# Performance work log

Measured on AMD Instinct MI355X. Metric: run time of the kernel, lower is better.

The kernel has to match this reference:

```python
import jax, jax.numpy as jnp
import numpy as np

N, E, F, ED, H, G = 100000, 400000, 143, 6, 128, 4096
NL = 3   # num_layers -> NL-1 atom GATConv layers
NT = 2   # num_timesteps


def leaky(v):
    return jnp.where(v >= 0, v, 0.01 * v)  # torch default negative_slope=0.01


def gru_cell(xin, hid, Wi, Wh, bi, bh):
    # torch.nn.GRUCell, gate order r,z,n
    gi = xin @ Wi.T + bi
    gh = hid @ Wh.T + bh
    ir, iz, inn = jnp.split(gi, 3, axis=-1)
    hr, hz, hn = jnp.split(gh, 3, axis=-1)
    r = jax.nn.sigmoid(ir + hr)
    z = jax.nn.sigmoid(iz + hz)
    n = jnp.tanh(inn + r * hn)
    return (1.0 - z) * n + z * hid


def seg_softmax(a, seg, num):
    m = jax.ops.segment_max(a, seg, num_segments=num)
    m = jnp.where(jnp.isfinite(m), m, 0.0)
    e = jnp.exp(a - m[seg])
    s = jax.ops.segment_sum(e, seg, num_segments=num)
    return e / (s[seg] + 1e-16)


def afp_forward(x, edge_attr, lin1_W, lin1_b, gc_lin1_W, gc_att_l, gc_att_r,
                gc_lin2_W, gc_bias, gru0_Wi, gru0_Wh, gru0_bi, gru0_bh,
                atom_W, atom_att_src, atom_att_dst, atom_bias,
                atom_gru_Wi, atom_gru_Wh, atom_gru_bi, atom_gru_bh,
                mol_W, mol_att_src, mol_att_dst, mol_bias,
                mol_gru_Wi, mol_gru_Wh, mol_gru_bi, mol_gru_bh,
                lin2_W, lin2_b, cls_W1, cls_b1, cls_W2, cls_b2,
                edge_index, batch, num_graphs):
    src, dst = edge_index[0], edge_index[1]
    Nn = x.shape[0]
    # lin1 + leaky_relu
    x0 = leaky(x @ lin1_W.T + lin1_b)                                  # [N,H]
    # GATEConv (edge-feature gated attention)
    t = leaky(jnp.concatenate([x0[src], edge_attr], axis=-1) @ gc_lin1_W.T)  # [E,H]
    alpha = leaky(t @ gc_att_l + (x0 @ gc_att_r)[dst])                 # [E]
    alpha = seg_softmax(alpha, dst, Nn)
    x2 = x0 @ gc_lin2_W.T
    agg = jax.ops.segment_sum(x2[src] * alpha[:, None], dst, num_segments=Nn) + gc_bias
    h = jax.nn.elu(agg)
    xh = jax.nn.relu(gru_cell(h, x0, gru0_Wi, gru0_Wh, gru0_bi, gru0_bh))
    # atom GATConv layers (single head, no self loops, slope 0.01)
    for l in range(atom_W.shape[0]):
        xl = xh @ atom_W[l].T                                          # [N,H]
        a = leaky((xl @ atom_att_src[l])[src] + (xl @ atom_att_dst[l])[dst])
        a = seg_softmax(a, dst, Nn)
        agg = jax.ops.segment_sum(xl[src] * a[:, None], dst, num_segments=Nn) + atom_bias[l]
        h = jax.nn.elu(agg)
        xh = jax.nn.relu(gru_cell(h, xh, atom_gru_Wi[l], atom_gru_Wh[l], atom_gru_bi[l], atom_gru_bh[l]))
    # molecule readout: bipartite GATConv node->graph + GRU, NT timesteps
    out = jax.nn.relu(jax.ops.segment_sum(xh, batch, num_segments=num_graphs))  # [G,H]
    xm = xh @ mol_W.T
    a_src = xm @ mol_att_src                                           # [N]
    for _ in range(NT):
        om = out @ mol_W.T
        a = leaky(a_src + (om @ mol_att_dst)[batch])
        a = seg_softmax(a, batch, num_graphs)
        agg = jax.ops.segment_sum(xm * a[:, None], batch, num_segments=num_graphs) + mol_bias
        h = jax.nn.elu(agg)
        out = jax.nn.relu(gru_cell(h, out, mol_gru_Wi, mol_gru_Wh, mol_gru_bi, mol_gru_bh))
    emb = out @ lin2_W.T + lin2_b                                      # [G,H]
    y = jax.nn.relu(emb @ cls_W1.T + cls_b1) @ cls_W2.T + cls_b2       # [G,1]
    return y[:, 0]


def setup_inputs():
    key = jax.random.key(0)
    ks = iter(jax.random.split(key, 64))
    def rn(shape, s=0.08):
        return jax.random.normal(next(ks), shape, dtype=jnp.float32) * s
    return dict(
        x=jax.random.normal(next(ks), (N, F), dtype=jnp.float32),
        edge_attr=jax.random.normal(next(ks), (E, ED), dtype=jnp.float32),
        lin1_W=rn((H, F)), lin1_b=rn((H,)),
        gc_lin1_W=rn((H, H + ED)), gc_att_l=rn((H,)), gc_att_r=rn((H,)),
        gc_lin2_W=rn((H, H)), gc_bias=rn((H,)),
        gru0_Wi=rn((3 * H, H)), gru0_Wh=rn((3 * H, H)), gru0_bi=rn((3 * H,)), gru0_bh=rn((3 * H,)),
        atom_W=rn((NL - 1, H, H)), atom_att_src=rn((NL - 1, H)), atom_att_dst=rn((NL - 1, H)), atom_bias=rn((NL - 1, H)),
        atom_gru_Wi=rn((NL - 1, 3 * H, H)), atom_gru_Wh=rn((NL - 1, 3 * H, H)),
        atom_gru_bi=rn((NL - 1, 3 * H)), atom_gru_bh=rn((NL - 1, 3 * H)),
        mol_W=rn((H, H)), mol_att_src=rn((H,)), mol_att_dst=rn((H,)), mol_bias=rn((H,)),
        mol_gru_Wi=rn((3 * H, H)), mol_gru_Wh=rn((3 * H, H)), mol_gru_bi=rn((3 * H,)), mol_gru_bh=rn((3 * H,)),
        lin2_W=rn((H, H)), lin2_b=rn((H,)),
        cls_W1=rn((64, H)), cls_b1=rn((64,)), cls_W2=rn((1, 64)), cls_b2=rn((1,)),
        edge_index=jax.random.randint(next(ks), (2, E), 0, N),
        batch=jnp.sort(jax.random.randint(next(ks), (N,), 0, G)),
        num_graphs=G,
    )


def reference(x, edge_attr, lin1_W, lin1_b, gc_lin1_W, gc_att_l, gc_att_r,
              gc_lin2_W, gc_bias, gru0_Wi, gru0_Wh, gru0_bi, gru0_bh,
              atom_W, atom_att_src, atom_att_dst, atom_bias,
              atom_gru_Wi, atom_gru_Wh, atom_gru_bi, atom_gru_bh,
              mol_W, mol_att_src, mol_att_dst, mol_bias,
              mol_gru_Wi, mol_gru_Wh, mol_gru_bi, mol_gru_bh,
              lin2_W, lin2_b, cls_W1, cls_b1, cls_W2, cls_b2,
              edge_index, batch, num_graphs):
    return afp_forward(x, edge_attr, lin1_W, lin1_b, gc_lin1_W, gc_att_l, gc_att_r,
                       gc_lin2_W, gc_bias, gru0_Wi, gru0_Wh, gru0_bi, gru0_bh,
                       atom_W, atom_att_src, atom_att_dst, atom_bias,
                       atom_gru_Wi, atom_gru_Wh, atom_gru_bi, atom_gru_bh,
                       mol_W, mol_att_src, mol_att_dst, mol_bias,
                       mol_gru_Wi, mol_gru_Wh, mol_gru_bi, mol_gru_bh,
                       lin2_W, lin2_b, cls_W1, cls_b1, cls_W2, cls_b2,
                       edge_index, batch, num_graphs)
```

## Files before the change

kernel.cpp:

```cpp
#include <hip/hip_runtime.h>

#define NND 100000
#define NED 400000
#define FEAT 143
#define FEATP 160
#define EDIM 6
#define H 128
#define NG 4096
#define NBS 391

typedef __attribute__((ext_vector_type(8))) short bf8;
typedef __attribute__((ext_vector_type(4))) float f4;

__device__ __forceinline__ float b2f(unsigned short u){
  unsigned int x = ((unsigned int)u) << 16;
  return __builtin_bit_cast(float, x);
}
__device__ __forceinline__ unsigned short f2b(float f){
  unsigned int u = __builtin_bit_cast(unsigned int, f);
  u = u + 0x7fffu + ((u >> 16) & 1u);
  return (unsigned short)(u >> 16);
}
__device__ __forceinline__ float lk(float v){ return v >= 0.f ? v : 0.01f*v; }
__device__ __forceinline__ float eluf(float v){ return v > 0.f ? v : __expf(v) - 1.f; }
__device__ __forceinline__ float sgm(float v){ return 1.f/(1.f + __expf(-v)); }
__device__ __forceinline__ float wsum(float v){
  #pragma unroll
  for(int o=32;o>0;o>>=1) v += __shfl_xor(v,o);
  return v;
}
__device__ __forceinline__ bf8 cvt8(const float* p){
  f4 a = *(const f4*)p;
  f4 b = *(const f4*)(p+4);
  bf8 t;
  t[0]=(short)f2b(a[0]); t[1]=(short)f2b(a[1]); t[2]=(short)f2b(a[2]); t[3]=(short)f2b(a[3]);
  t[4]=(short)f2b(b[0]); t[5]=(short)f2b(b[1]); t[6]=(short)f2b(b[2]); t[7]=(short)f2b(b[3]);
  return t;
}

__global__ __launch_bounds__(256) void k_wfrag(const float* __restrict__ src, int lds, int srcK,
                                               unsigned short* __restrict__ dst, int NT, int KB){
  int i = blockIdx.x*256 + threadIdx.x;
  int total = NT*KB*512;
  if (i >= total) return;
  int j = i & 7, lane = (i>>3) & 63, kb = (i>>9) % KB, nt = i/(KB*512);
  int n = nt*16 + (lane & 15), k = kb*32 + (lane>>4)*8 + j;
  dst[i] = (k < srcK) ? f2b(src[(size_t)n*lds + k]) : (unsigned short)0;
}

__global__ __launch_bounds__(256) void k_hist(const int* __restrict__ ei, int* __restrict__ deg){
  int e = blockIdx.x*256 + threadIdx.x;
  if (e < NED) atomicAdd(&deg[ei[NED + e]], 1);
}
__global__ __launch_bounds__(256) void k_scan1(const int* __restrict__ deg, int* __restrict__ off, int* __restrict__ bsum){
  __shared__ int s[256];
  int i = blockIdx.x*256 + threadIdx.x;
  int v = (i < NND) ? deg[i] : 0;
  s[threadIdx.x] = v; __syncthreads();
  for(int o=1;o<256;o<<=1){
    int t = 0; if (threadIdx.x >= o) t = s[threadIdx.x - o];
    __syncthreads(); s[threadIdx.x] += t; __syncthreads();
  }
  if (i < NND) off[i] = s[threadIdx.x] - v;
  if (threadIdx.x == 255) bsum[blockIdx.x] = s[255];
}
__global__ __launch_bounds__(512) void k_scan2(int* __restrict__ bsum){
  __shared__ int s[512];
  int t = threadIdx.x;
  int v = (t < NBS) ? bsum[t] : 0;
  s[t] = v; __syncthreads();
  for(int o=1;o<512;o<<=1){
    int x = 0; if (t >= o) x = s[t - o];
    __syncthreads(); s[t] += x; __syncthreads();
  }
  if (t < NBS) bsum[t] = s[t] - v;
  if (t == 511) bsum[NBS] = s[511];
}
__global__ __launch_bounds__(256) void k_scan3(int* __restrict__ off, const int* __restrict__ bsum, int* __restrict__ cursor){
  int i = blockIdx.x*256 + threadIdx.x;
  if (i < NND){
    int v = off[i] + bsum[blockIdx.x];
    off[i] = v; cursor[i] = v;
  }
  if (i == 0) off[NND] = bsum[NBS];
}
__global__ __launch_bounds__(256) void k_scatter(const int* __restrict__ ei, int* __restrict__ cursor, int* __restrict__ perm){
  int e = blockIdx.x*256 + threadIdx.x;
  if (e < NED){
    int p = atomicAdd(&cursor[ei[NED + e]], 1);
    perm[p] = e;
  }
}
__global__ __launch_bounds__(256) void k_gstart(const int* __restrict__ batch, int* __restrict__ goff){
  int i = blockIdx.x*256 + threadIdx.x;
  if (i >= NND) return;
  int bi = batch[i];
  int bp = (i > 0) ? batch[i-1] : -1;
  for(int g = bp+1; g <= bi; g++) goff[g] = i;
  if (i == NND-1) for(int g = bi+1; g <= NG; g++) goff[g] = NND;
}

__global__ __launch_bounds__(256) void k_padx(const float* __restrict__ x, unsigned short* __restrict__ xp){
  int r = blockIdx.x*4 + (threadIdx.x >> 6);
  int lane = threadIdx.x & 63;
  if (r >= NND) return;
  for(int i = lane; i < FEATP; i += 64)
    xp[(size_t)r*FEATP + i] = (i < FEAT) ? f2b(x[(size_t)r*FEAT + i]) : (unsigned short)0;
}

template<int KB, int RT, bool ABF16, bool BIAS, int ACT, bool OBF16>
__global__ __launch_bounds__(256) void k_gemm(const void* __restrict__ Ap, int lda,
        const unsigned short* __restrict__ Wf,
        const float* __restrict__ bias, void* __restrict__ Cp, int M)
{
  int tid = threadIdx.x, wave = tid >> 6, lane = tid & 63;
  int m = lane & 15, quad = lane >> 4;
  int r0 = blockIdx.x * (16*RT);
  bf8 a[RT][KB];
  #pragma unroll
  for(int rt=0; rt<RT; rt++){
    int row = r0 + rt*16 + m;
    if (ABF16){
      const unsigned short* base = (const unsigned short*)Ap + (size_t)row*lda + quad*8;
      #pragma unroll
      for(int kb=0;kb<KB;kb++) a[rt][kb] = *(const bf8*)(base + kb*32);
    } else {
      const float* base = (const float*)Ap + (size_t)row*lda + quad*8;
      #pragma unroll
      for(int kb=0;kb<KB;kb++) a[rt][kb] = cvt8(base + kb*32);
    }
  }
  #pragma unroll
  for(int ct=0;ct<2;ct++){
    int nt = wave*2 + ct;
    int n = nt*16 + m;
    const bf8* wf = (const bf8*)Wf + (size_t)nt*KB*64;
    bf8 b[KB];
    #pragma unroll
    for(int kb=0;kb<KB;kb++) b[kb] = wf[kb*64 + lane];
    float bv = BIAS ? bias[n] : 0.f;
    #pragma unroll
    for(int rt=0;rt<RT;rt++){
      f4 acc = {0.f,0.f,0.f,0.f};
      #pragma unroll
      for(int kb=0;kb<KB;kb++)
        acc = __builtin_amdgcn_mfma_f32_16x16x32_bf16(a[rt][kb], b[kb], acc, 0, 0, 0);
      #pragma unroll
      for(int i=0;i<4;i++){
        int row = r0 + rt*16 + quad*4 + i;
        if (row < M){
          float v = acc[i] + bv;
          if (ACT == 1) v = lk(v);
          if (OBF16) ((unsigned short*)Cp)[(size_t)row*H + n] = f2b(v);
          else       ((float*)Cp)[(size_t)row*H + n] = v;
        }
      }
    }
  }
}

__global__ __launch_bounds__(256) void k_gru(const float* __restrict__ Xin,
      const float* __restrict__ Hid, float* __restrict__ Out,
      const unsigned short* __restrict__ Wif, const unsigned short* __restrict__ Whf,
      const float* __restrict__ bi, const float* __restrict__ bh_)
{
  int tid = threadIdx.x, wave = tid >> 6, lane = tid & 63;
  int m = lane & 15, quad = lane >> 4;
  int r0 = blockIdx.x * 32;
  bf8 ax[2][4], ah[2][4];
  #pragma unroll
  for(int rt=0;rt<2;rt++){
    const float* xb = Xin + (size_t)(r0+rt*16+m)*H + quad*8;
    const float* hb = Hid + (size_t)(r0+rt*16+m)*H + quad*8;
    #pragma unroll
    for(int kb=0;kb<4;kb++){
      ax[rt][kb] = cvt8(xb + kb*32);
      ah[rt][kb] = cvt8(hb + kb*32);
    }
  }
  __syncthreads();
  f4 rg[2][2], ng[2][2];
  #pragma unroll
  for(int c=0;c<2;c++){
    int nt = wave*2 + c;
    const bf8* wi = (const bf8*)Wif + (size_t)nt*256;
    const bf8* wh = (const bf8*)Whf + (size_t)nt*256;
    int col = nt*16 + m;
    float bb = bi[col] + bh_[col];
    #pragma unroll
    for(int rt=0;rt<2;rt++){
      f4 acc = {0.f,0.f,0.f,0.f};
      #pragma unroll
      for(int kb=0;kb<4;kb++){
        acc = __builtin_amdgcn_mfma_f32_16x16x32_bf16(ax[rt][kb], wi[kb*64+lane], acc,0,0,0);
        acc = __builtin_amdgcn_mfma_f32_16x16x32_bf16(ah[rt][kb], wh[kb*64+lane], acc,0,0,0);
      }
      #pragma unroll
      for(int i=0;i<4;i++) rg[c][rt][i] = sgm(acc[i] + bb);
    }
  }
  #pragma unroll
  for(int c=0;c<2;c++){
    int nt = 16 + wave*2 + c;
    const bf8* wi = (const bf8*)Wif + (size_t)nt*256;
    const bf8* wh = (const bf8*)Whf + (size_t)nt*256;
    int col = (wave*2+c)*16 + m;
    float bin_ = bi[col+256], bhn_ = bh_[col+256];
    #pragma unroll
    for(int rt=0;rt<2;rt++){
      f4 a1 = {0.f,0.f,0.f,0.f}, a2 = {0.f,0.f,0.f,0.f};
      #pragma unroll
      for(int kb=0;kb<4;kb++){
        a1 = __builtin_amdgcn_mfma_f32_16x16x32_bf16(ax[rt][kb], wi[kb*64+lane], a1,0,0,0);
        a2 = __builtin_amdgcn_mfma_f32_16x16x32_bf16(ah[rt][kb], wh[kb*64+lane], a2,0,0,0);
      }
      #pragma unroll
      for(int i=0;i<4;i++)
        ng[c][rt][i] = tanhf(a1[i] + bin_ + rg[c][rt][i]*(a2[i] + bhn_));
    }
  }
  #pragma unroll
  for(int c=0;c<2;c++){
    int nt = 8 + wave*2 + c;
    const bf8* wi = (const bf8*)Wif + (size_t)nt*256;
    const bf8* wh = (const bf8*)Whf + (size_t)nt*256;
    int col = (wave*2+c)*16 + m;
    float bb = bi[col+128] + bh_[col+128];
    #pragma unroll
    for(int rt=0;rt<2;rt++){
      f4 acc = {0.f,0.f,0.f,0.f};
      #pragma unroll
      for(int kb=0;kb<4;kb++){
        acc = __builtin_amdgcn_mfma_f32_16x16x32_bf16(ax[rt][kb], wi[kb*64+lane], acc,0,0,0);
        acc = __builtin_amdgcn_mfma_f32_16x16x32_bf16(ah[rt][kb], wh[kb*64+lane], acc,0,0,0);
      }
      #pragma unroll
      for(int i=0;i<4;i++){
        float zg = sgm(acc[i] + bb);
        int row = r0 + rt*16 + quad*4 + i;
        float hv = Hid[(size_t)row*H + col];
        float o = (1.f - zg)*ng[c][rt][i] + zg*hv;
        Out[(size_t)row*H + col] = fmaxf(o, 0.f);
      }
    }
  }
}

template<bool ABF16, bool TWO>
__global__ __launch_bounds__(256) void k_rowdot(const void* __restrict__ Ap,
    const float* __restrict__ v1, const float* __restrict__ v2,
    float* __restrict__ o1, float* __restrict__ o2, int M)
{
  int idx = blockIdx.x*4 + (threadIdx.x >> 6);
  if (idx >= M) return;
  int lane = threadIdx.x & 63;
  int h0 = lane*2;
  float a0, a1;
  if (ABF16){
    unsigned int q = *(const unsigned int*)((const unsigned short*)Ap + (size_t)idx*H + h0);
    a0 = b2f((unsigned short)(q & 0xffffu)); a1 = b2f((unsigned short)(q >> 16));
  } else {
    const float* p = (const float*)Ap + (size_t)idx*H + h0;
    a0 = p[0]; a1 = p[1];
  }
  float p1 = a0*v1[h0] + a1*v1[h0+1];
  p1 = wsum(p1);
  if (lane == 0) o1[idx] = p1;
  if (TWO){
    float p2 = a0*v2[h0] + a1*v2[h0+1];
    p2 = wsum(p2);
    if (lane == 0) o2[idx] = p2;
  }
}

__global__ __launch_bounds__(256) void k_gate_agg(
   const int* __restrict__ ei, const float* __restrict__ eattr,
   const float* __restrict__ gcW, const float* __restrict__ attl,
   const float* __restrict__ r, const unsigned short* __restrict__ u,
   const unsigned short* __restrict__ x2, const float* __restrict__ gbias,
   const int* __restrict__ off, const int* __restrict__ perm,
   float* __restrict__ hout)
{
  __shared__ float W1e_s[H*EDIM];
  int tid = threadIdx.x;
  for(int i=tid;i<H*EDIM;i+=256) W1e_s[i] = gcW[(i/EDIM)*(H+EDIM) + H + (i%EDIM)];
  __syncthreads();
  int wave = tid >> 6, lane = tid & 63;
  int grp = lane >> 4, sub = lane & 15;
  int n = blockIdx.x*4 + wave;
  if (n >= NND) return;
  int o0 = off[n], deg = off[n+1] - o0;
  int c0 = sub*8;
  float attl8[8];
  #pragma unroll
  for(int c=0;c<8;c++) attl8[c] = attl[c0+c];
  float rn = r[n];
  float mx = -3.4e38f, S = 0.f;
  float acc[8] = {0,0,0,0,0,0,0,0};
  for(int base=0; base<deg; base+=64){
    int cnt = min(deg - base, 64);
    int e_l = 0, s_l = 0;
    if (lane < cnt){ e_l = perm[o0 + base + lane]; s_l = ei[e_l]; }
    #pragma unroll 1
    for(int k=0;k<16;k++){
      int l = grp + k*4;
      if (l >= cnt) break;
      int e = __shfl(e_l, l);
      int s = __shfl(s_l, l);
      const float* ep = eattr + (size_t)e*EDIM;
      bf8 uv = *(const bf8*)(u  + (size_t)s*H + c0);
      bf8 xv = *(const bf8*)(x2 + (size_t)s*H + c0);
      float p = 0.f;
      #pragma unroll
      for(int c=0;c<8;c++){
        float ve = 0.f;
        #pragma unroll
        for(int j=0;j<EDIM;j++) ve += ep[j] * W1e_s[(c0+c)*EDIM + j];
        float t = lk(b2f((unsigned short)uv[c]) + ve);
        p += t * attl8[c];
      }
      #pragma unroll
      for(int o=1;o<16;o<<=1) p += __shfl_xor(p, o);
      float araw = lk(p + rn);
      float mnew = fmaxf(mx, araw);
      float sc = __expf(mx - mnew);
      float w  = __expf(araw - mnew);
      S = S*sc + w;
      #pragma unroll
      for(int c=0;c<8;c++) acc[c] = acc[c]*sc + w*b2f((unsigned short)xv[c]);
      mx = mnew;
    }
  }
  #pragma unroll
  for(int o=16;o<64;o<<=1){
    float mo = __shfl_xor(mx, o);
    float So = __shfl_xor(S, o);
    float mnew = fmaxf(mx, mo);
    float sa = __expf(mx - mnew), sb = __expf(mo - mnew);
    S = S*sa + So*sb;
    #pragma unroll
    for(int c=0;c<8;c++){
      float ao = __shfl_xor(acc[c], o);
      acc[c] = acc[c]*sa + ao*sb;
    }
    mx = mnew;
  }
  float inv = 1.f/(S + 1e-16f);
  if (grp == 0){
    #pragma unroll
    for(int c=0;c<8;c++)
      hout[(size_t)n*H + c0 + c] = eluf(acc[c]*inv + gbias[c0+c]);
  }
}

__global__ __launch_bounds__(256) void k_atom_agg(
    const int* __restrict__ ei, const float* __restrict__ s1, const float* __restrict__ s2,
    const unsigned short* __restrict__ xl, const float* __restrict__ abias,
    const int* __restrict__ off, const int* __restrict__ perm,
    float* __restrict__ hout)
{
  int tid = threadIdx.x, wave = tid >> 6, lane = tid & 63;
  int grp = lane >> 4, sub = lane & 15;
  int n = blockIdx.x*4 + wave;
  if (n >= NND) return;
  int o0 = off[n], deg = off[n+1] - o0;
  int c0 = sub*8;
  float s2n = s2[n];
  float mx = -3.4e38f, S = 0.f;
  float acc[8] = {0,0,0,0,0,0,0,0};
  for(int base=0; base<deg; base+=64){
    int cnt = min(deg - base, 64);
    int s_l = 0; float ar_l = 0.f;
    if (lane < cnt){ int e = perm[o0 + base + lane]; s_l = ei[e]; ar_l = lk(s1[s_l] + s2n); }
    #pragma unroll 1
    for(int k=0;k<16;k++){
      int l = grp + k*4;
      if (l >= cnt) break;
      int s = __shfl(s_l, l);
      float araw = __shfl(ar_l, l);
      bf8 xv = *(const bf8*)(xl + (size_t)s*H + c0);
      float mnew = fmaxf(mx, araw);
      float sc = __expf(mx - mnew);
      float w  = __expf(araw - mnew);
      S = S*sc + w;
      #pragma unroll
      for(int c=0;c<8;c++) acc[c] = acc[c]*sc + w*b2f((unsigned short)xv[c]);
      mx = mnew;
    }
  }
  #pragma unroll
  for(int o=16;o<64;o<<=1){
    float mo = __shfl_xor(mx, o);
    float So = __shfl_xor(S, o);
    float mnew = fmaxf(mx, mo);
    float sa = __expf(mx - mnew), sb = __expf(mo - mnew);
    S = S*sa + So*sb;
    #pragma unroll
    for(int c=0;c<8;c++){
      float ao = __shfl_xor(acc[c], o);
      acc[c] = acc[c]*sa + ao*sb;
    }
    mx = mnew;
  }
  float inv = 1.f/(S + 1e-16f);
  if (grp == 0){
    #pragma unroll
    for(int c=0;c<8;c++)
      hout[(size_t)n*H + c0 + c] = eluf(acc[c]*inv + abias[c0+c]);
  }
}

__global__ __launch_bounds__(256) void k_seg0(const float* __restrict__ xh, const int* __restrict__ goff,
                                              float* __restrict__ outg)
{
  int g = blockIdx.x*4 + (threadIdx.x >> 6);
  if (g >= NG) return;
  int lane = threadIdx.x & 63;
  int gs = goff[g], ge = goff[g+1];
  int h0 = lane*2;
  float a0 = 0.f, a1 = 0.f;
  for(int n=gs;n<ge;n++){
    const float* p = xh + (size_t)n*H + h0;
    a0 += p[0]; a1 += p[1];
  }
  outg[(size_t)g*H + h0]   = fmaxf(a0, 0.f);
  outg[(size_t)g*H + h0+1] = fmaxf(a1, 0.f);
}

__global__ __launch_bounds__(256) void k_mol_agg(const float* __restrict__ asrc, const float* __restrict__ d,
    const unsigned short* __restrict__ xm, const int* __restrict__ goff,
    const float* __restrict__ mbias, float* __restrict__ hmol)
{
  int tid = threadIdx.x, wave = tid >> 6, lane = tid & 63;
  int grp = lane >> 4, sub = lane & 15;
  int g = blockIdx.x*4 + wave;
  if (g >= NG) return;
  int gs = goff[g], num = goff[g+1] - gs;
  int c0 = sub*8;
  float dg = d[g];
  float mx = -3.4e38f, S = 0.f;
  float acc[8] = {0,0,0,0,0,0,0,0};
  for(int base=0; base<num; base+=64){
    int cnt = min(num - base, 64);
    float ar_l = 0.f;
    if (lane < cnt) ar_l = lk(asrc[gs + base + lane] + dg);
    #pragma unroll 1
    for(int k=0;k<16;k++){
      int l = grp + k*4;
      if (l >= cnt) break;
      float araw = __shfl(ar_l, l);
      int node = gs + base + l;
      bf8 xv = *(const bf8*)(xm + (size_t)node*H + c0);
      float mnew = fmaxf(mx, araw);
      float sc = __expf(mx - mnew);
      float w  = __expf(araw - mnew);
      S = S*sc + w;
      #pragma unroll
      for(int c=0;c<8;c++) acc[c] = acc[c]*sc + w*b2f((unsigned short)xv[c]);
      mx = mnew;
    }
  }
  #pragma unroll
  for(int o=16;o<64;o<<=1){
    float mo = __shfl_xor(mx, o);
    float So = __shfl_xor(S, o);
    float mnew = fmaxf(mx, mo);
    float sa = __expf(mx - mnew), sb = __expf(mo - mnew);
    S = S*sa + So*sb;
    #pragma unroll
    for(int c=0;c<8;c++){
      float ao = __shfl_xor(acc[c], o);
      acc[c] = acc[c]*sa + ao*sb;
    }
    mx = mnew;
  }
  float inv = 1.f/(S + 1e-16f);
  if (grp == 0){
    #pragma unroll
    for(int c=0;c<8;c++)
      hmol[(size_t)g*H + c0 + c] = eluf(acc[c]*inv + mbias[c0+c]);
  }
}

__global__ __launch_bounds__(256) void k_cls(const float* __restrict__ emb,
   const float* __restrict__ W1, const float* __restrict__ b1,
   const float* __restrict__ W2, const float* __restrict__ b2,
   float* __restrict__ outp)
{
  __shared__ float W1t[H*64];
  int tid = threadIdx.x;
  for(int i=tid;i<64*H;i+=256){
    int l = i >> 7, hh = i & 127;
    W1t[hh*64 + l] = W1[i];
  }
  __syncthreads();
  int wave = tid >> 6, lane = tid & 63;
  int g = blockIdx.x*4 + wave;
  if (g >= NG) return;
  const float* er = emb + (size_t)g*H;
  float acc = 0.f;
  for(int hh=0;hh<H;hh++) acc += er[hh] * W1t[hh*64 + lane];
  float hid = fmaxf(acc + b1[lane], 0.f);
  float p = hid * W2[lane];
  p = wsum(p);
  if (lane == 0) outp[g] = p + b2[0];
}

extern "C" void kernel_launch(void* const* d_in, const int* in_sizes, int n_in,
                              void* d_out, int out_size, void* d_ws, size_t ws_size,
                              hipStream_t stream)
{
  const float* x      = (const float*)d_in[0];
  const float* eattr  = (const float*)d_in[1];
  const float* lin1W  = (const float*)d_in[2];
  const float* lin1b  = (const float*)d_in[3];
  const float* gcW    = (const float*)d_in[4];
  const float* gcatl  = (const float*)d_in[5];
  const float* gcatr  = (const float*)d_in[6];
  const float* gcW2   = (const float*)d_in[7];
  const float* gcb    = (const float*)d_in[8];
  const float* g0Wi   = (const float*)d_in[9];
  const float* g0Wh   = (const float*)d_in[10];
  const float* g0bi   = (const float*)d_in[11];
  const float* g0bh   = (const float*)d_in[12];
  const float* aW     = (const float*)d_in[13];
  const float* aas    = (const float*)d_in[14];
  const float* aad    = (const float*)d_in[15];
  const float* ab     = (const float*)d_in[16];
  const float* agWi   = (const float*)d_in[17];
  const float* agWh   = (const float*)d_in[18];
  const float* agbi   = (const float*)d_in[19];
  const float* agbh   = (const float*)d_in[20];
  const float* mW     = (const float*)d_in[21];
  const float* mas    = (const float*)d_in[22];
  const float* mad    = (const float*)d_in[23];
  const float* mb     = (const float*)d_in[24];
  const float* mgWi   = (const float*)d_in[25];
  const float* mgWh   = (const float*)d_in[26];
  const float* mgbi   = (const float*)d_in[27];
  const float* mgbh   = (const float*)d_in[28];
  const float* l2W    = (const float*)d_in[29];
  const float* l2b    = (const float*)d_in[30];
  const float* cW1    = (const float*)d_in[31];
  const float* cb1    = (const float*)d_in[32];
  const float* cW2    = (const float*)d_in[33];
  const float* cb2    = (const float*)d_in[34];
  const int* ei    = (const int*)d_in[35];
  const int* batch = (const int*)d_in[36];
  float* outp = (float*)d_out;

  char* p = (char*)d_ws;
  auto alloc = [&](size_t sz)->void*{ void* q = (void*)p; p += (sz + 511) & ~(size_t)511; return q; };
  float* x0            = (float*)alloc((size_t)NND*H*4);
  unsigned short* bu   = (unsigned short*)alloc((size_t)NND*H*2);
  unsigned short* bx2  = (unsigned short*)alloc((size_t)NND*H*2);
  float* xh            = (float*)alloc((size_t)NND*H*4);
  float* bh            = (float*)alloc((size_t)NND*H*4);
  unsigned short* xm   = (unsigned short*)x0;
  unsigned short* xp   = (unsigned short*)bh;
  float* rbuf          = (float*)alloc((size_t)NND*4);
  float* s1            = (float*)alloc((size_t)NND*4);
  float* s2            = (float*)alloc((size_t)NND*4);
  float* asrc          = (float*)alloc((size_t)NND*4);
  int* deg             = (int*)alloc((size_t)NND*4);
  int* off             = (int*)alloc((size_t)(NND+1)*4);
  int* cursor          = (int*)alloc((size_t)NND*4);
  int* perm            = (int*)alloc((size_t)NED*4);
  int* bsum            = (int*)alloc((size_t)(NBS+1)*4);
  int* goff            = (int*)alloc((size_t)(NG+1)*4);
  float* outg          = (float*)alloc((size_t)NG*H*4);
  float* hmol          = (float*)alloc((size_t)NG*H*4);
  float* om            = (float*)alloc((size_t)NG*H*4);
  float* emb           = (float*)alloc((size_t)NG*H*4);
  float* dgb           = (float*)alloc((size_t)NG*4);
  unsigned short* wp     = (unsigned short*)alloc((size_t)8*5*512*2);
  unsigned short* gcWnb  = (unsigned short*)alloc((size_t)H*H*2);
  unsigned short* gcW2b  = (unsigned short*)alloc((size_t)H*H*2);
  unsigned short* g0Wib  = (unsigned short*)alloc((size_t)3*H*H*2);
  unsigned short* g0Whb  = (unsigned short*)alloc((size_t)3*H*H*2);
  unsigned short* aWb    = (unsigned short*)alloc((size_t)2*H*H*2);
  unsigned short* agWib  = (unsigned short*)alloc((size_t)2*3*H*H*2);
  unsigned short* agWhb  = (unsigned short*)alloc((size_t)2*3*H*H*2);
  unsigned short* mWb    = (unsigned short*)alloc((size_t)H*H*2);
  unsigned short* l2Wb   = (unsigned short*)alloc((size_t)H*H*2);
  unsigned short* mgWib  = (unsigned short*)alloc((size_t)3*H*H*2);
  unsigned short* mgWhb  = (unsigned short*)alloc((size_t)3*H*H*2);

  const int HH = H*H, H3H = 3*H*H;
  k_wfrag<<<80 ,256,0,stream>>>(lin1W, FEAT, FEAT, wp, 8, 5);
  k_wfrag<<<64 ,256,0,stream>>>(gcW, H+EDIM, H, gcWnb, 8, 4);
  k_wfrag<<<64 ,256,0,stream>>>(gcW2, H, H, gcW2b, 8, 4);
  k_wfrag<<<192,256,0,stream>>>(g0Wi, H, H, g0Wib, 24, 4);
  k_wfrag<<<192,256,0,stream>>>(g0Wh, H, H, g0Whb, 24, 4);
  for(int l=0;l<2;l++){
    k_wfrag<<<64 ,256,0,stream>>>(aW + (size_t)l*HH, H, H, aWb + (size_t)l*HH, 8, 4);
    k_wfrag<<<192,256,0,stream>>>(agWi + (size_t)l*H3H, H, H, agWib + (size_t)l*H3H, 24, 4);
    k_wfrag<<<192,256,0,stream>>>(agWh + (size_t)l*H3H, H, H, agWhb + (size_t)l*H3H, 24, 4);
  }
  k_wfrag<<<64 ,256,0,stream>>>(mW, H, H, mWb, 8, 4);
  k_wfrag<<<64 ,256,0,stream>>>(l2W, H, H, l2Wb, 8, 4);
  k_wfrag<<<192,256,0,stream>>>(mgWi, H, H, mgWib, 24, 4);
  k_wfrag<<<192,256,0,stream>>>(mgWh, H, H, mgWhb, 24, 4);

  hipMemsetAsync(deg, 0, (size_t)NND*4, stream);
  k_hist<<<1563,256,0,stream>>>(ei, deg);
  k_scan1<<<NBS,256,0,stream>>>(deg, off, bsum);
  k_scan2<<<1,512,0,stream>>>(bsum);
  k_scan3<<<NBS,256,0,stream>>>(off, bsum, cursor);
  k_scatter<<<1563,256,0,stream>>>(ei, cursor, perm);
  k_gstart<<<NBS,256,0,stream>>>(batch, goff);

  const int GB = (NND + 63)/64;
  k_padx<<<25000,256,0,stream>>>(x, xp);
  k_gemm<5,4,true,true,1,false><<<GB,256,0,stream>>>(xp, FEATP, wp, lin1b, x0, NND);

  k_rowdot<false,false><<<25000,256,0,stream>>>(x0, gcatr, nullptr, rbuf, nullptr, NND);
  k_gemm<4,4,false,false,0,true><<<GB,256,0,stream>>>(x0, H, gcWnb, nullptr, bu, NND);
  k_gemm<4,4,false,false,0,true><<<GB,256,0,stream>>>(x0, H, gcW2b, nullptr, bx2, NND);
  k_gate_agg<<<25000,256,0,stream>>>(ei, eattr, gcW, gcatl, rbuf, bu, bx2, gcb, off, perm, bh);
  k_gru<<<NND/32,256,0,stream>>>(bh, x0, xh, g0Wib, g0Whb, g0bi, g0bh);

  for(int l=0;l<2;l++){
    k_gemm<4,4,false,false,0,true><<<GB,256,0,stream>>>(xh, H, aWb + (size_t)l*HH, nullptr, bu, NND);
    k_rowdot<true,true><<<25000,256,0,stream>>>(bu, aas + l*H, aad + l*H, s1, s2, NND);
    k_atom_agg<<<25000,256,0,stream>>>(ei, s1, s2, bu, ab + l*H, off, perm, bh);
    k_gru<<<NND/32,256,0,stream>>>(bh, xh, xh, agWib + (size_t)l*H3H, agWhb + (size_t)l*H3H,
                                   agbi + l*3*H, agbh + l*3*H);
  }

  k_seg0<<<NG/4,256,0,stream>>>(xh, goff, outg);
  k_gemm<4,4,false,false,0,true><<<GB,256,0,stream>>>(xh, H, mWb, nullptr, xm, NND);
  k_rowdot<true,false><<<25000,256,0,stream>>>(xm, mas, nullptr, asrc, nullptr, NND);
  for(int t=0;t<2;t++){
    k_gemm<4,4,false,false,0,false><<<(NG+63)/64,256,0,stream>>>(outg, H, mWb, nullptr, om, NG);
    k_rowdot<false,false><<<NG/4,256,0,stream>>>(om, mad, nullptr, dgb, nullptr, NG);
    k_mol_agg<<<NG/4,256,0,stream>>>(asrc, dgb, xm, goff, mb, hmol);
    k_gru<<<NG/32,256,0,stream>>>(hmol, outg, outg, mgWib, mgWhb, mgbi, mgbh);
  }

  k_gemm<4,4,false,true,0,false><<<(NG+63)/64,256,0,stream>>>(outg, H, l2Wb, l2b, emb, NG);
  k_cls<<<NG/4,256,0,stream>>>(emb, cW1, cb1, cW2, cb2, outp);
}
```

Measured before the change: 1.105 ms.

## Fuse attention row-dots into GEMM epilogues and merge gate GEMMs interleaved

The separate row-dot kernels are removed. Their dot products are computed inside the GEMM epilogue using shuffle reductions and atomicAdd into output buffers, which are zeroed by one up-front memset. The two GATE GEMMs (u and x2) become one kernel that writes an interleaved [N,256] bf16 buffer, so the gather in gate_agg loads a contiguous 32-byte chunk per source row. The edge weights move from shared memory into per-lane registers. This cuts kernel launches and re-reads of the N×H activations, at the cost of atomics, extra register pressure, and order-dependent float summation.

```diff
diff --git a/kernel.cpp b/kernel.cpp
--- a/kernel.cpp
+++ b/kernel.cpp
@@ -108,10 +108,12 @@
     xp[(size_t)r*FEATP + i] = (i < FEAT) ? f2b(x[(size_t)r*FEAT + i]) : (unsigned short)0;
 }
 
-template<int KB, int RT, bool ABF16, bool BIAS, int ACT, bool OBF16>
+template<int KB, int RT, bool ABF16, bool BIAS, int ACT, bool OBF16, int DOT>
 __global__ __launch_bounds__(256) void k_gemm(const void* __restrict__ Ap, int lda,
         const unsigned short* __restrict__ Wf,
-        const float* __restrict__ bias, void* __restrict__ Cp, int M)
+        const float* __restrict__ bias, void* __restrict__ Cp, int M,
+        const float* __restrict__ v1, const float* __restrict__ v2,
+        float* __restrict__ o1, float* __restrict__ o2)
 {
   int tid = threadIdx.x, wave = tid >> 6, lane = tid & 63;
   int m = lane & 15, quad = lane >> 4;
@@ -129,6 +131,13 @@
       #pragma unroll
       for(int kb=0;kb<KB;kb++) a[rt][kb] = cvt8(base + kb*32);
     }
+  }
+  float d1[RT][4], d2[RT][4];
+  if (DOT >= 1){
+    #pragma unroll
+    for(int rt=0;rt<RT;rt++)
+      #pragma unroll
+      for(int i=0;i<4;i++){ d1[rt][i] = 0.f; if (DOT==2) d2[rt][i] = 0.f; }
   }
   #pragma unroll
   for(int ct=0;ct<2;ct++){
@@ -139,6 +148,8 @@
     #pragma unroll
     for(int kb=0;kb<KB;kb++) b[kb] = wf[kb*64 + lane];
     float bv = BIAS ? bias[n] : 0.f;
+    float vv1 = (DOT>=1) ? v1[n] : 0.f;
+    float vv2 = (DOT==2) ? v2[n] : 0.f;
     #pragma unroll
     for(int rt=0;rt<RT;rt++){
       f4 acc = {0.f,0.f,0.f,0.f};
@@ -148,11 +159,73 @@
       #pragma unroll
       for(int i=0;i<4;i++){
         int row = r0 + rt*16 + quad*4 + i;
+        float v = acc[i] + bv;
+        if (ACT == 1) v = lk(v);
+        if (DOT >= 1){ d1[rt][i] += v*vv1; if (DOT==2) d2[rt][i] += v*vv2; }
         if (row < M){
-          float v = acc[i] + bv;
-          if (ACT == 1) v = lk(v);
           if (OBF16) ((unsigned short*)Cp)[(size_t)row*H + n] = f2b(v);
           else       ((float*)Cp)[(size_t)row*H + n] = v;
+        }
+      }
+    }
+  }
+  if (DOT >= 1){
+    #pragma unroll
+    for(int rt=0;rt<RT;rt++){
+      #pragma unroll
+      for(int i=0;i<4;i++){
+        float dd = d1[rt][i];
+        #pragma unroll
+        for(int o=1;o<16;o<<=1) dd += __shfl_xor(dd, o);
+        int row = r0 + rt*16 + quad*4 + i;
+        if (m == 0 && row < M) atomicAdd(&o1[row], dd);
+        if (DOT == 2){
+          float ee = d2[rt][i];
+          #pragma unroll
+          for(int o=1;o<16;o<<=1) ee += __shfl_xor(ee, o);
+          if (m == 0 && row < M) atomicAdd(&o2[row], ee);
+        }
+      }
+    }
+  }
+}
+
+__global__ __launch_bounds__(256) void k_gemm2(const float* __restrict__ A,
+        const unsigned short* __restrict__ Wf1, const unsigned short* __restrict__ Wf2,
+        unsigned short* __restrict__ ux, int M)
+{
+  int tid = threadIdx.x, wave = tid >> 6, lane = tid & 63;
+  int m = lane & 15, quad = lane >> 4;
+  int r0 = blockIdx.x * 64;
+  bf8 a[4][4];
+  #pragma unroll
+  for(int rt=0; rt<4; rt++){
+    const float* base = A + (size_t)(r0 + rt*16 + m)*H + quad*8;
+    #pragma unroll
+    for(int kb=0;kb<4;kb++) a[rt][kb] = cvt8(base + kb*32);
+  }
+  #pragma unroll
+  for(int ws=0; ws<2; ws++){
+    const unsigned short* Wf = ws ? Wf2 : Wf1;
+    #pragma unroll
+    for(int ct=0;ct<2;ct++){
+      int nt = wave*2 + ct;
+      int n = nt*16 + m;
+      const bf8* wf = (const bf8*)Wf + (size_t)nt*256;
+      bf8 b[4];
+      #pragma unroll
+      for(int kb=0;kb<4;kb++) b[kb] = wf[kb*64 + lane];
+      int pos = (n>>3)*16 + ws*8 + (n&7);
+      #pragma unroll
+      for(int rt=0;rt<4;rt++){
+        f4 acc = {0.f,0.f,0.f,0.f};
+        #pragma unroll
+        for(int kb=0;kb<4;kb++)
+          acc = __builtin_amdgcn_mfma_f32_16x16x32_bf16(a[rt][kb], b[kb], acc, 0, 0, 0);
+        #pragma unroll
+        for(int i=0;i<4;i++){
+          int row = r0 + rt*16 + quad*4 + i;
+          if (row < M) ux[(size_t)row*256 + pos] = f2b(acc[i]);
         }
       }
     }
@@ -246,54 +319,30 @@
   }
 }
 
-template<bool ABF16, bool TWO>
-__global__ __launch_bounds__(256) void k_rowdot(const void* __restrict__ Ap,
-    const float* __restrict__ v1, const float* __restrict__ v2,
-    float* __restrict__ o1, float* __restrict__ o2, int M)
-{
-  int idx = blockIdx.x*4 + (threadIdx.x >> 6);
-  if (idx >= M) return;
-  int lane = threadIdx.x & 63;
-  int h0 = lane*2;
-  float a0, a1;
-  if (ABF16){
-    unsigned int q = *(const unsigned int*)((const unsigned short*)Ap + (size_t)idx*H + h0);
-    a0 = b2f((unsigned short)(q & 0xffffu)); a1 = b2f((unsigned short)(q >> 16));
-  } else {
-    const float* p = (const float*)Ap + (size_t)idx*H + h0;
-    a0 = p[0]; a1 = p[1];
-  }
-  float p1 = a0*v1[h0] + a1*v1[h0+1];
-  p1 = wsum(p1);
-  if (lane == 0) o1[idx] = p1;
-  if (TWO){
-    float p2 = a0*v2[h0] + a1*v2[h0+1];
-    p2 = wsum(p2);
-    if (lane == 0) o2[idx] = p2;
-  }
-}
-
 __global__ __launch_bounds__(256) void k_gate_agg(
    const int* __restrict__ ei, const float* __restrict__ eattr,
    const float* __restrict__ gcW, const float* __restrict__ attl,
-   const float* __restrict__ r, const unsigned short* __restrict__ u,
-   const unsigned short* __restrict__ x2, const float* __restrict__ gbias,
+   const float* __restrict__ r, const unsigned short* __restrict__ ux,
+   const float* __restrict__ gbias,
    const int* __restrict__ off, const int* __restrict__ perm,
    float* __restrict__ hout)
 {
-  __shared__ float W1e_s[H*EDIM];
   int tid = threadIdx.x;
-  for(int i=tid;i<H*EDIM;i+=256) W1e_s[i] = gcW[(i/EDIM)*(H+EDIM) + H + (i%EDIM)];
-  __syncthreads();
   int wave = tid >> 6, lane = tid & 63;
   int grp = lane >> 4, sub = lane & 15;
   int n = blockIdx.x*4 + wave;
   if (n >= NND) return;
+  int c0 = sub*8;
+  float W1e[48];
+  #pragma unroll
+  for(int c=0;c<8;c++)
+    #pragma unroll
+    for(int j=0;j<EDIM;j++)
+      W1e[c*EDIM+j] = gcW[(size_t)(c0+c)*(H+EDIM) + H + j];
+  float attl8[8];
+  #pragma unroll
+  for(int c=0;c<8;c++) attl8[c] = attl[c0+c];
   int o0 = off[n], deg = off[n+1] - o0;
-  int c0 = sub*8;
-  float attl8[8];
-  #pragma unroll
-  for(int c=0;c<8;c++) attl8[c] = attl[c0+c];
   float rn = r[n];
   float mx = -3.4e38f, S = 0.f;
   float acc[8] = {0,0,0,0,0,0,0,0};
@@ -308,14 +357,15 @@
       int e = __shfl(e_l, l);
       int s = __shfl(s_l, l);
       const float* ep = eattr + (size_t)e*EDIM;
-      bf8 uv = *(const bf8*)(u  + (size_t)s*H + c0);
-      bf8 xv = *(const bf8*)(x2 + (size_t)s*H + c0);
+      const unsigned short* rowp = ux + (size_t)s*256 + sub*16;
+      bf8 uv = *(const bf8*)rowp;
+      bf8 xv = *(const bf8*)(rowp + 8);
       float p = 0.f;
       #pragma unroll
       for(int c=0;c<8;c++){
         float ve = 0.f;
         #pragma unroll
-        for(int j=0;j<EDIM;j++) ve += ep[j] * W1e_s[(c0+c)*EDIM + j];
+        for(int j=0;j<EDIM;j++) ve += ep[j] * W1e[c*EDIM + j];
         float t = lk(b2f((unsigned short)uv[c]) + ve);
         p += t * attl8[c];
       }
@@ -552,16 +602,22 @@
   char* p = (char*)d_ws;
   auto alloc = [&](size_t sz)->void*{ void* q = (void*)p; p += (sz + 511) & ~(size_t)511; return q; };
   float* x0            = (float*)alloc((size_t)NND*H*4);
+  unsigned short* ux   = (unsigned short*)alloc((size_t)NND*256*2);
   unsigned short* bu   = (unsigned short*)alloc((size_t)NND*H*2);
-  unsigned short* bx2  = (unsigned short*)alloc((size_t)NND*H*2);
   float* xh            = (float*)alloc((size_t)NND*H*4);
   float* bh            = (float*)alloc((size_t)NND*H*4);
   unsigned short* xm   = (unsigned short*)x0;
   unsigned short* xp   = (unsigned short*)bh;
+  char* z0 = p;
   float* rbuf          = (float*)alloc((size_t)NND*4);
-  float* s1            = (float*)alloc((size_t)NND*4);
-  float* s2            = (float*)alloc((size_t)NND*4);
+  float* s1a           = (float*)alloc((size_t)NND*4);
+  float* s2a           = (float*)alloc((size_t)NND*4);
+  float* s1b           = (float*)alloc((size_t)NND*4);
+  float* s2b           = (float*)alloc((size_t)NND*4);
   float* asrc          = (float*)alloc((size_t)NND*4);
+  float* dg0           = (float*)alloc((size_t)NG*4);
+  float* dg1           = (float*)alloc((size_t)NG*4);
+  size_t zbytes = (size_t)(p - z0);
   int* deg             = (int*)alloc((size_t)NND*4);
   int* off             = (int*)alloc((size_t)(NND+1)*4);
   int* cursor          = (int*)alloc((size_t)NND*4);
@@ -572,7 +628,6 @@
   float* hmol          = (float*)alloc((size_t)NG*H*4);
   float* om            = (float*)alloc((size_t)NG*H*4);
   float* emb           = (float*)alloc((size_t)NG*H*4);
-  float* dgb           = (float*)alloc((size_t)NG*4);
   unsigned short* wp     = (unsigned short*)alloc((size_t)8*5*512*2);
   unsigned short* gcWnb  = (unsigned short*)alloc((size_t)H*H*2);
   unsigned short* gcW2b  = (unsigned short*)alloc((size_t)H*H*2);
@@ -602,6 +657,7 @@
   k_wfrag<<<192,256,0,stream>>>(mgWi, H, H, mgWib, 24, 4);
   k_wfrag<<<192,256,0,stream>>>(mgWh, H, H, mgWhb, 24, 4);
 
+  hipMemsetAsync(z0, 0, zbytes, stream);
   hipMemsetAsync(deg, 0, (size_t)NND*4, stream);
   k_hist<<<1563,256,0,stream>>>(ei, deg);
   k_scan1<<<NBS,256,0,stream>>>(deg, off, bsum);
@@ -612,32 +668,34 @@
 
   const int GB = (NND + 63)/64;
   k_padx<<<25000,256,0,stream>>>(x, xp);
-  k_gemm<5,4,true,true,1,false><<<GB,256,0,stream>>>(xp, FEATP, wp, lin1b, x0, NND);
-
-  k_rowdot<false,false><<<25000,256,0,stream>>>(x0, gcatr, nullptr, rbuf, nullptr, NND);
-  k_gemm<4,4,false,false,0,true><<<GB,256,0,stream>>>(x0, H, gcWnb, nullptr, bu, NND);
-  k_gemm<4,4,false,false,0,true><<<GB,256,0,stream>>>(x0, H, gcW2b, nullptr, bx2, NND);
-  k_gate_agg<<<25000,256,0,stream>>>(ei, eattr, gcW, gcatl, rbuf, bu, bx2, gcb, off, perm, bh);
+  k_gemm<5,4,true,true,1,false,1><<<GB,256,0,stream>>>(xp, FEATP, wp, lin1b, x0, NND,
+                                                       gcatr, nullptr, rbuf, nullptr);
+  k_gemm2<<<GB,256,0,stream>>>(x0, gcWnb, gcW2b, ux, NND);
+  k_gate_agg<<<25000,256,0,stream>>>(ei, eattr, gcW, gcatl, rbuf, ux, gcb, off, perm, bh);
   k_gru<<<NND/32,256,0,stream>>>(bh, x0, xh, g0Wib, g0Whb, g0bi, g0bh);
 
+  float* s1l[2] = {s1a, s1b};
+  float* s2l[2] = {s2a, s2b};
   for(int l=0;l<2;l++){
-    k_gemm<4,4,false,false,0,true><<<GB,256,0,stream>>>(xh, H, aWb + (size_t)l*HH, nullptr, bu, NND);
-    k_rowdot<true,true><<<25000,256,0,stream>>>(bu, aas + l*H, aad + l*H, s1, s2, NND);
-    k_atom_agg<<<25000,256,0,stream>>>(ei, s1, s2, bu, ab + l*H, off, perm, bh);
+    k_gemm<4,4,false,false,0,true,2><<<GB,256,0,stream>>>(xh, H, aWb + (size_t)l*HH, nullptr, bu, NND,
+                                                          aas + l*H, aad + l*H, s1l[l], s2l[l]);
+    k_atom_agg<<<25000,256,0,stream>>>(ei, s1l[l], s2l[l], bu, ab + l*H, off, perm, bh);
     k_gru<<<NND/32,256,0,stream>>>(bh, xh, xh, agWib + (size_t)l*H3H, agWhb + (size_t)l*H3H,
                                    agbi + l*3*H, agbh + l*3*H);
   }
 
   k_seg0<<<NG/4,256,0,stream>>>(xh, goff, outg);
-  k_gemm<4,4,false,false,0,true><<<GB,256,0,stream>>>(xh, H, mWb, nullptr, xm, NND);
-  k_rowdot<true,false><<<25000,256,0,stream>>>(xm, mas, nullptr, asrc, nullptr, NND);
+  k_gemm<4,4,false,false,0,true,1><<<GB,256,0,stream>>>(xh, H, mWb, nullptr, xm, NND,
+                                                        mas, nullptr, asrc, nullptr);
+  float* dgt[2] = {dg0, dg1};
   for(int t=0;t<2;t++){
-    k_gemm<4,4,false,false,0,false><<<(NG+63)/64,256,0,stream>>>(outg, H, mWb, nullptr, om, NG);
-    k_rowdot<false,false><<<NG/4,256,0,stream>>>(om, mad, nullptr, dgb, nullptr, NG);
-    k_mol_agg<<<NG/4,256,0,stream>>>(asrc, dgb, xm, goff, mb, hmol);
+    k_gemm<4,4,false,false,0,false,1><<<(NG+63)/64,256,0,stream>>>(outg, H, mWb, nullptr, om, NG,
+                                                                   mad, nullptr, dgt[t], nullptr);
+    k_mol_agg<<<NG/4,256,0,stream>>>(asrc, dgt[t], xm, goff, mb, hmol);
     k_gru<<<NG/32,256,0,stream>>>(hmol, outg, outg, mgWib, mgWhb, mgbi, mgbh);
   }
 
-  k_gemm<4,4,false,true,0,false><<<(NG+63)/64,256,0,stream>>>(outg, H, l2Wb, l2b, emb, NG);
+  k_gemm<4,4,false,true,0,false,0><<<(NG+63)/64,256,0,stream>>>(outg, H, l2Wb, l2b, emb, NG,
+                                                                nullptr, nullptr, nullptr, nullptr);
   k_cls<<<NG/4,256,0,stream>>>(emb, cW1, cb1, cW2, cb2, outp);
 }
```

Measured after the change: 1.106 ms. Within noise of the previous version (+0.0%).
